# Optimization experiments

Hardware: AMD Instinct MI355X
Metric: run time of the kernel (lower is better)

Reference implementation:

```python
import jax, jax.numpy as jnp
import numpy as np

N_NODES = 100000
N_EDGES = 1600000
IN_FEAT = 128
HEADS = 4
OUT_FEAT = 16
ALPHA = 0.2  # LeakyReLU negative slope


def setup_inputs() -> dict:
    key = jax.random.key(0)
    k1, k2, k3, k4, k5 = jax.random.split(key, 5)
    x = jax.random.normal(k1, (N_NODES, IN_FEAT), dtype=jnp.float32)
    edge_index = jax.random.randint(k2, (2, N_EDGES), 0, N_NODES, dtype=jnp.int64)
    # xavier_uniform with gain=1.414
    gain = 1.414
    lim_W = gain * np.sqrt(6.0 / (IN_FEAT + HEADS * OUT_FEAT))
    W = jax.random.uniform(k3, (IN_FEAT, HEADS * OUT_FEAT), minval=-lim_W, maxval=lim_W, dtype=jnp.float32)
    lim_a = gain * np.sqrt(6.0 / (HEADS + OUT_FEAT))
    a_src = jax.random.uniform(k4, (HEADS, OUT_FEAT), minval=-lim_a, maxval=lim_a, dtype=jnp.float32)
    a_dst = jax.random.uniform(k5, (HEADS, OUT_FEAT), minval=-lim_a, maxval=lim_a, dtype=jnp.float32)
    return {"x": x, "edge_index": edge_index, "W": W, "a_src": a_src, "a_dst": a_dst}


def reference(x, edge_index, W, a_src, a_dst):
    N = x.shape[0]
    H, F = a_src.shape
    src, dst = edge_index[0], edge_index[1]

    h = (x @ W).reshape(N, H, F)                 # [N, H, F]
    att_src = jnp.sum(h * a_src, axis=-1)        # [N, H]
    att_dst = jnp.sum(h * a_dst, axis=-1)        # [N, H]

    e = jax.nn.leaky_relu(att_src[src] + att_dst[dst], negative_slope=ALPHA)  # [E, H]

    # segment softmax over edges grouped by dst
    e_max = jax.ops.segment_max(e, dst, num_segments=N)   # [N, H]
    e_max = jnp.where(jnp.isfinite(e_max), e_max, 0.0)    # nodes with no in-edges
    ex = jnp.exp(e - e_max[dst])                           # [E, H]
    denom = jax.ops.segment_sum(ex, dst, num_segments=N)  # [N, H]
    alpha = ex / (denom[dst] + 1e-16)                      # [E, H]
    # dropout: inference mode (training=False) -> identity

    messages = h[src] * alpha[:, :, None]                  # [E, H, F]
    out = jax.ops.segment_sum(messages, dst, num_segments=N)  # [N, H, F]

    out = out.reshape(N, H * F)  # concat=True
    out = jax.nn.elu(out)
    return out
```

## Files before the change

kernel.cpp:

```cpp
#include <hip/hip_runtime.h>


#define NEG_SLOPE 0.2f
#define BSHIFT 9
#define BNODES 512
#define CH 2048
#define BCB 512
#define QSHIFT 7
#define QNODES 128
#define QCAP 2816

typedef __bf16 bf16x8 __attribute__((ext_vector_type(8)));
typedef float  f32x4  __attribute__((ext_vector_type(4)));

static __device__ __forceinline__ unsigned f2b(float f) {
    union { float f; unsigned u; } v; v.f = f;
    return (v.u + 0x7fffu + ((v.u >> 16) & 1u)) >> 16;
}
static __device__ __forceinline__ float u2f(unsigned u) {
    union { unsigned u32; float f; } v; v.u32 = u; return v.f;
}

__global__ __launch_bounds__(256) void gemm_att_kernel(
    const float* __restrict__ x,
    const float* __restrict__ W,
    const float* __restrict__ a_src,
    const float* __restrict__ a_dst,
    unsigned short* __restrict__ h_out,
    float* __restrict__ att_s_o,
    float* __restrict__ att_d_o,
    const int* __restrict__ dst,
    int* __restrict__ bucketCount,
    int N, int E, int gemmBlocks)
{
    __shared__ bf16x8 Wswz[20][64];
    __shared__ int c[256];
    int t = threadIdx.x;

    if (blockIdx.x >= gemmBlocks) {
        int bid = blockIdx.x - gemmBlocks;
        c[t] = 0;
        __syncthreads();
        for (int e = bid * 256 + t; e < E; e += BCB * 256)
            atomicAdd(&c[dst[e] >> BSHIFT], 1);
        __syncthreads();
        if (c[t]) atomicAdd(&bucketCount[t], c[t]);
        return;
    }

    for (int i = t; i < 8192; i += 256) {
        int k = i >> 6, n = i & 63;
        __bf16* dp = (__bf16*)&Wswz[((n >> 4) << 2) | (k >> 5)]
                                   [(((k >> 3) & 3) << 4) | (n & 15)];
        dp[k & 7] = (__bf16)W[i];
    }
    for (int i = t; i < 1024; i += 256) {
        int k = i >> 3, c7 = i & 7;
        int hd = c7 & 3;
        const float* aa = (c7 < 4) ? a_src : a_dst;
        float sum = 0.f;
        #pragma unroll
        for (int f = 0; f < 16; ++f)
            sum = fmaf(W[k * 64 + hd * 16 + f], aa[hd * 16 + f], sum);
        __bf16* dp = (__bf16*)&Wswz[16 + (k >> 5)][(((k >> 3) & 3) << 4) | c7];
        dp[k & 7] = (__bf16)sum;
        __bf16* dz = (__bf16*)&Wswz[16 + (k >> 5)][(((k >> 3) & 3) << 4) | (8 + c7)];
        dz[k & 7] = (__bf16)0.f;
    }
    __syncthreads();

    int wave = t >> 6;
    int lane = t & 63;
    int col = lane & 15, quad = lane >> 4;
    int node_base = (blockIdx.x * 4 + wave) * 16;
    int arow = min(node_base + col, N - 1);
    const float* xp = x + arow * 128;

    bf16x8 af[4];
    #pragma unroll
    for (int tt = 0; tt < 4; ++tt) {
        float4 xa = *(const float4*)(xp + tt * 32 + quad * 8);
        float4 xb = *(const float4*)(xp + tt * 32 + quad * 8 + 4);
        bf16x8 f;
        f[0] = (__bf16)xa.x; f[1] = (__bf16)xa.y;
        f[2] = (__bf16)xa.z; f[3] = (__bf16)xa.w;
        f[4] = (__bf16)xb.x; f[5] = (__bf16)xb.y;
        f[6] = (__bf16)xb.z; f[7] = (__bf16)xb.w;
        af[tt] = f;
    }

    f32x4 acc[4], accA;
    #pragma unroll
    for (int cb = 0; cb < 4; ++cb) {
        acc[cb] = (f32x4){0.f, 0.f, 0.f, 0.f};
        #pragma unroll
        for (int tt = 0; tt < 4; ++tt)
            acc[cb] = __builtin_amdgcn_mfma_f32_16x16x32_bf16(
                af[tt], Wswz[(cb << 2) | tt][lane], acc[cb], 0, 0, 0);
    }
    accA = (f32x4){0.f, 0.f, 0.f, 0.f};
    #pragma unroll
    for (int tt = 0; tt < 4; ++tt)
        accA = __builtin_amdgcn_mfma_f32_16x16x32_bf16(
            af[tt], Wswz[16 + tt][lane], accA, 0, 0, 0);

    #pragma unroll
    for (int cb = 0; cb < 4; ++cb) {
        #pragma unroll
        for (int r = 0; r < 4; ++r) {
            int node = node_base + quad * 4 + r;
            if (node < N)
                h_out[node * 64 + cb * 16 + col] = (unsigned short)f2b(acc[cb][r]);
        }
    }
    if (col < 8) {
        #pragma unroll
        for (int r = 0; r < 4; ++r) {
            int node = node_base + quad * 4 + r;
            if (node < N) {
                if (col < 4) att_s_o[(node << 2) | col] = accA[r];
                else         att_d_o[(node << 2) | (col - 4)] = accA[r];
            }
        }
    }
}

__global__ __launch_bounds__(256) void bscatter_kernel(
    const int* __restrict__ src, const int* __restrict__ dst,
    const int* __restrict__ bucketCount,
    int* __restrict__ bucketCursor, int* __restrict__ pairs, int nb, int E)
{
    __shared__ int cnt[256], lo[256], gpos[256], cur[256], sm[256], gbc[256];
    __shared__ int2 staged[CH];
    int t = threadIdx.x;
    int base = blockIdx.x * CH;
    int nloc = min(CH, E - base);

    cnt[t] = 0;
    gbc[t] = (t < nb) ? bucketCount[t] : 0;
    __syncthreads();
    for (int i = t; i < nloc; i += 256)
        atomicAdd(&cnt[dst[base + i] >> BSHIFT], 1);
    __syncthreads();

    int v = cnt[t];
    sm[t] = v;
    __syncthreads();
    #pragma unroll
    for (int off = 1; off < 256; off <<= 1) {
        int u = (t >= off) ? sm[t - off] : 0;
        __syncthreads();
        sm[t] += u;
        __syncthreads();
    }
    lo[t] = sm[t] - v;
    cur[t] = lo[t];
    __syncthreads();

    int g = gbc[t];
    sm[t] = g;
    __syncthreads();
    #pragma unroll
    for (int off = 1; off < 256; off <<= 1) {
        int u = (t >= off) ? sm[t - off] : 0;
        __syncthreads();
        sm[t] += u;
        __syncthreads();
    }
    gpos[t] = (v > 0) ? (sm[t] - g) + atomicAdd(&bucketCursor[t], v) : 0;
    __syncthreads();

    for (int i = t; i < nloc; i += 256) {
        int d = dst[base + i];
        int s = src[base + i];
        int b = d >> BSHIFT;
        int k = atomicAdd(&cur[b], 1);
        staged[k] = make_int2((s << BSHIFT) | (d & (BNODES - 1)), b);
    }
    __syncthreads();

    for (int i = t; i < nloc; i += 256) {
        int2 p = staged[i];
        pairs[gpos[p.y] + (i - lo[p.y])] = p.x;
    }
}

__global__ __launch_bounds__(256, 8) void bucket_csr_agg_kernel(
    const int* __restrict__ pairs,
    const int* __restrict__ bucketCount,
    const float* __restrict__ att_s,
    const float* __restrict__ att_d,
    const unsigned short* __restrict__ hmat,
    float* __restrict__ out,
    int nb, int N)
{
    __shared__ int sorted[QCAP];
    __shared__ int cnt[QNODES], rs[QNODES + 1], cur[QNODES], sm[QNODES];
    __shared__ int gbc[256], gsm[256];
    __shared__ float attd[QNODES * 4];

    int blk = blockIdx.x, t = threadIdx.x;
    int b = blk >> 2, quar = blk & 3;
    int node_lo = (b << BSHIFT) + (quar << QSHIFT);
    if (node_lo >= N) return;
    int nn = min(QNODES, N - node_lo);

    { int g = (t < nb) ? bucketCount[t] : 0; gbc[t] = g; gsm[t] = g; }
    if (t < QNODES) cnt[t] = 0;
    __syncthreads();
    #pragma unroll
    for (int off = 1; off < 256; off <<= 1) {
        int u = (t >= off) ? gsm[t - off] : 0;
        __syncthreads();
        gsm[t] += u;
        __syncthreads();
    }
    int ebase = gsm[b] - gbc[b];
    int ecnt  = gbc[b];

    for (int i = t; i < (nn << 2); i += 256)
        attd[i] = att_d[(node_lo << 2) + i];

    for (int i = t; i < ecnt; i += 256) {
        int dl = pairs[ebase + i] & (BNODES - 1);
        if ((dl >> QSHIFT) == quar)
            atomicAdd(&cnt[dl & (QNODES - 1)], 1);
    }
    __syncthreads();

    int v = (t < QNODES) ? cnt[t] : 0;
    if (t < QNODES) sm[t] = v;
    __syncthreads();
    #pragma unroll
    for (int off = 1; off < QNODES; off <<= 1) {
        int u = (t >= off && t < QNODES) ? sm[t - off] : 0;
        __syncthreads();
        if (t < QNODES) sm[t] += u;
        __syncthreads();
    }
    if (t < QNODES) { int x = sm[t] - v; rs[t] = x; cur[t] = x; }
    if (t == 0) rs[QNODES] = 0;
    __syncthreads();
    if (t == 0) rs[QNODES] = (QNODES <= nn) ? sm[QNODES - 1] : sm[QNODES - 1];
    __syncthreads();

    for (int i = t; i < ecnt; i += 256) {
        int p = pairs[ebase + i];
        int dl = p & (BNODES - 1);
        if ((dl >> QSHIFT) == quar) {
            int k = atomicAdd(&cur[dl & (QNODES - 1)], 1);
            if (k < QCAP) sorted[k] = p >> BSHIFT;
        }
    }
    __syncthreads();

    int q = t & 7;
    int h = q >> 1;

    for (int pass = 0; pass < 4; ++pass) {
        int node = (pass << 5) + (t >> 3);
        if (node >= nn) continue;
        int beg = rs[node];
        int deg = rs[node + 1] - beg;
        float ad = attd[(node << 2) | h];

        float a0 = 0.f, a1 = 0.f, a2 = 0.f, a3 = 0.f;
        float a4 = 0.f, a5 = 0.f, a6 = 0.f, a7 = 0.f, l = 0.f;
        int d1 = deg - 1;
        for (int e0 = 0; e0 < deg; e0 += 4) {
            int s0 = sorted[beg + min(e0 + 0, d1)];
            int s1 = sorted[beg + min(e0 + 1, d1)];
            int s2 = sorted[beg + min(e0 + 2, d1)];
            int s3 = sorted[beg + min(e0 + 3, d1)];
            float t0 = att_s[(s0 << 2) | h];
            float t1 = att_s[(s1 << 2) | h];
            float t2 = att_s[(s2 << 2) | h];
            float t3 = att_s[(s3 << 2) | h];
            uint4 hp0 = *(const uint4*)(hmat + (s0 << 6) + (q << 3));
            uint4 hp1 = *(const uint4*)(hmat + (s1 << 6) + (q << 3));
            uint4 hp2 = *(const uint4*)(hmat + (s2 << 6) + (q << 3));
            uint4 hp3 = *(const uint4*)(hmat + (s3 << 6) + (q << 3));
            float av0 = t0 + ad; av0 = fmaxf(av0, NEG_SLOPE * av0);
            float av1 = t1 + ad; av1 = fmaxf(av1, NEG_SLOPE * av1);
            float av2 = t2 + ad; av2 = fmaxf(av2, NEG_SLOPE * av2);
            float av3 = t3 + ad; av3 = fmaxf(av3, NEG_SLOPE * av3);
            float w0 = __expf(av0);
            float w1 = (e0 + 1 < deg) ? __expf(av1) : 0.f;
            float w2 = (e0 + 2 < deg) ? __expf(av2) : 0.f;
            float w3 = (e0 + 3 < deg) ? __expf(av3) : 0.f;
            l += w0 + w1 + w2 + w3;
            a0 = fmaf(w0, u2f(hp0.x << 16), a0);
            a1 = fmaf(w0, u2f(hp0.x & 0xffff0000u), a1);
            a2 = fmaf(w0, u2f(hp0.y << 16), a2);
            a3 = fmaf(w0, u2f(hp0.y & 0xffff0000u), a3);
            a4 = fmaf(w0, u2f(hp0.z << 16), a4);
            a5 = fmaf(w0, u2f(hp0.z & 0xffff0000u), a5);
            a6 = fmaf(w0, u2f(hp0.w << 16), a6);
            a7 = fmaf(w0, u2f(hp0.w & 0xffff0000u), a7);
            a0 = fmaf(w1, u2f(hp1.x << 16), a0);
            a1 = fmaf(w1, u2f(hp1.x & 0xffff0000u), a1);
            a2 = fmaf(w1, u2f(hp1.y << 16), a2);
            a3 = fmaf(w1, u2f(hp1.y & 0xffff0000u), a3);
            a4 = fmaf(w1, u2f(hp1.z << 16), a4);
            a5 = fmaf(w1, u2f(hp1.z & 0xffff0000u), a5);
            a6 = fmaf(w1, u2f(hp1.w << 16), a6);
            a7 = fmaf(w1, u2f(hp1.w & 0xffff0000u), a7);
            a0 = fmaf(w2, u2f(hp2.x << 16), a0);
            a1 = fmaf(w2, u2f(hp2.x & 0xffff0000u), a1);
            a2 = fmaf(w2, u2f(hp2.y << 16), a2);
            a3 = fmaf(w2, u2f(hp2.y & 0xffff0000u), a3);
            a4 = fmaf(w2, u2f(hp2.z << 16), a4);
            a5 = fmaf(w2, u2f(hp2.z & 0xffff0000u), a5);
            a6 = fmaf(w2, u2f(hp2.w << 16), a6);
            a7 = fmaf(w2, u2f(hp2.w & 0xffff0000u), a7);
            a0 = fmaf(w3, u2f(hp3.x << 16), a0);
            a1 = fmaf(w3, u2f(hp3.x & 0xffff0000u), a1);
            a2 = fmaf(w3, u2f(hp3.y << 16), a2);
            a3 = fmaf(w3, u2f(hp3.y & 0xffff0000u), a3);
            a4 = fmaf(w3, u2f(hp3.z << 16), a4);
            a5 = fmaf(w3, u2f(hp3.z & 0xffff0000u), a5);
            a6 = fmaf(w3, u2f(hp3.w << 16), a6);
            a7 = fmaf(w3, u2f(hp3.w & 0xffff0000u), a7);
        }

        float rl = 1.0f / (l + 1e-16f);
        float4 v0, v1;
        v0.x = a0 * rl; v0.x = (v0.x > 0.f) ? v0.x : (__expf(v0.x) - 1.f);
        v0.y = a1 * rl; v0.y = (v0.y > 0.f) ? v0.y : (__expf(v0.y) - 1.f);
        v0.z = a2 * rl; v0.z = (v0.z > 0.f) ? v0.z : (__expf(v0.z) - 1.f);
        v0.w = a3 * rl; v0.w = (v0.w > 0.f) ? v0.w : (__expf(v0.w) - 1.f);
        v1.x = a4 * rl; v1.x = (v1.x > 0.f) ? v1.x : (__expf(v1.x) - 1.f);
        v1.y = a5 * rl; v1.y = (v1.y > 0.f) ? v1.y : (__expf(v1.y) - 1.f);
        v1.z = a6 * rl; v1.z = (v1.z > 0.f) ? v1.z : (__expf(v1.z) - 1.f);
        v1.w = a7 * rl; v1.w = (v1.w > 0.f) ? v1.w : (__expf(v1.w) - 1.f);
        float* op = out + ((size_t)(node_lo + node) << 6) + (q << 3);
        *(float4*)op = v0;
        *(float4*)(op + 4) = v1;
    }
}

extern "C" void kernel_launch(void* const* d_in, const int* in_sizes, int n_in,
                              void* d_out, int out_size, void* d_ws, size_t ws_size,
                              hipStream_t stream) {
    const float* x     = (const float*)d_in[0];
    const int*   ei    = (const int*)d_in[1];
    const float* W     = (const float*)d_in[2];
    const float* a_src = (const float*)d_in[3];
    const float* a_dst = (const float*)d_in[4];

    int N = in_sizes[0] / 128;
    int E = in_sizes[1] / 2;
    const int* src = ei;
    const int* dst = ei + E;
    int nb = (N + BNODES - 1) / BNODES;

    char* ws = (char*)d_ws;
    size_t off = 0;
    unsigned short* hmat = (unsigned short*)(ws + off); off += (size_t)N * 64 * 2;
    float* att_s = (float*)(ws + off);  off += (size_t)N * 4 * 4;
    float* att_d = (float*)(ws + off);  off += (size_t)N * 4 * 4;
    int* pairs    = (int*)(ws + off);   off += (size_t)E * 4;
    int* bucketCount  = (int*)(ws + off); off += 256 * 4;
    int* bucketCursor = (int*)(ws + off); off += 256 * 4;

    hipMemsetAsync(bucketCount, 0, 512 * 4, stream);

    int gemmBlocks = (N + 63) / 64;
    gemm_att_kernel<<<gemmBlocks + BCB, 256, 0, stream>>>(
        x, W, a_src, a_dst, hmat, att_s, att_d, dst, bucketCount,
        N, E, gemmBlocks);

    int blocksS = (E + CH - 1) / CH;
    bscatter_kernel<<<blocksS, 256, 0, stream>>>(src, dst, bucketCount,
                                                 bucketCursor, pairs, nb, E);

    bucket_csr_agg_kernel<<<nb * 4, 256, 0, stream>>>(
        pairs, bucketCount, att_s, att_d, hmat, (float*)d_out, nb, N);
}
```

Measured before the change: 211.3 us.

## Split aggregation buckets into eighths and precompute bucket offsets in scatter

```diff
diff --git a/kernel.cpp b/kernel.cpp
--- a/kernel.cpp
+++ b/kernel.cpp
@@ -6,9 +6,9 @@
 #define BNODES 512
 #define CH 2048
 #define BCB 512
-#define QSHIFT 7
-#define QNODES 128
-#define QCAP 2816
+#define QSHIFT 6
+#define QNODES 64
+#define QCAP 1536
 
 typedef __bf16 bf16x8 __attribute__((ext_vector_type(8)));
 typedef float  f32x4  __attribute__((ext_vector_type(4)));
@@ -128,7 +128,8 @@
 __global__ __launch_bounds__(256) void bscatter_kernel(
     const int* __restrict__ src, const int* __restrict__ dst,
     const int* __restrict__ bucketCount,
-    int* __restrict__ bucketCursor, int* __restrict__ pairs, int nb, int E)
+    int* __restrict__ bucketCursor, int* __restrict__ pairs,
+    int* __restrict__ bbase, int nb, int E)
 {
     __shared__ int cnt[256], lo[256], gpos[256], cur[256], sm[256], gbc[256];
     __shared__ int2 staged[CH];
@@ -168,6 +169,10 @@
         __syncthreads();
     }
     gpos[t] = (v > 0) ? (sm[t] - g) + atomicAdd(&bucketCursor[t], v) : 0;
+    if (blockIdx.x == 0) {
+        bbase[t + 1] = sm[t];
+        if (t == 0) bbase[0] = 0;
+    }
     __syncthreads();
 
     for (int i = t; i < nloc; i += 256) {
@@ -187,43 +192,34 @@
 
 __global__ __launch_bounds__(256, 8) void bucket_csr_agg_kernel(
     const int* __restrict__ pairs,
-    const int* __restrict__ bucketCount,
+    const int* __restrict__ bbase,
     const float* __restrict__ att_s,
     const float* __restrict__ att_d,
     const unsigned short* __restrict__ hmat,
     float* __restrict__ out,
-    int nb, int N)
+    int N)
 {
     __shared__ int sorted[QCAP];
     __shared__ int cnt[QNODES], rs[QNODES + 1], cur[QNODES], sm[QNODES];
-    __shared__ int gbc[256], gsm[256];
     __shared__ float attd[QNODES * 4];
 
     int blk = blockIdx.x, t = threadIdx.x;
-    int b = blk >> 2, quar = blk & 3;
-    int node_lo = (b << BSHIFT) + (quar << QSHIFT);
+    int b = blk >> 3, s8 = blk & 7;
+    int node_lo = (b << BSHIFT) + (s8 << QSHIFT);
     if (node_lo >= N) return;
     int nn = min(QNODES, N - node_lo);
 
-    { int g = (t < nb) ? bucketCount[t] : 0; gbc[t] = g; gsm[t] = g; }
+    int ebase = bbase[b];
+    int ecnt  = bbase[b + 1] - ebase;
+
     if (t < QNODES) cnt[t] = 0;
-    __syncthreads();
-    #pragma unroll
-    for (int off = 1; off < 256; off <<= 1) {
-        int u = (t >= off) ? gsm[t - off] : 0;
-        __syncthreads();
-        gsm[t] += u;
-        __syncthreads();
-    }
-    int ebase = gsm[b] - gbc[b];
-    int ecnt  = gbc[b];
-
     for (int i = t; i < (nn << 2); i += 256)
         attd[i] = att_d[(node_lo << 2) + i];
+    __syncthreads();
 
     for (int i = t; i < ecnt; i += 256) {
         int dl = pairs[ebase + i] & (BNODES - 1);
-        if ((dl >> QSHIFT) == quar)
+        if ((dl >> QSHIFT) == s8)
             atomicAdd(&cnt[dl & (QNODES - 1)], 1);
     }
     __syncthreads();
@@ -238,16 +234,16 @@
         if (t < QNODES) sm[t] += u;
         __syncthreads();
     }
-    if (t < QNODES) { int x = sm[t] - v; rs[t] = x; cur[t] = x; }
-    if (t == 0) rs[QNODES] = 0;
-    __syncthreads();
-    if (t == 0) rs[QNODES] = (QNODES <= nn) ? sm[QNODES - 1] : sm[QNODES - 1];
+    if (t < QNODES) {
+        int x = sm[t] - v; rs[t] = x; cur[t] = x;
+        if (t == QNODES - 1) rs[QNODES] = sm[t];
+    }
     __syncthreads();
 
     for (int i = t; i < ecnt; i += 256) {
         int p = pairs[ebase + i];
         int dl = p & (BNODES - 1);
-        if ((dl >> QSHIFT) == quar) {
+        if ((dl >> QSHIFT) == s8) {
             int k = atomicAdd(&cur[dl & (QNODES - 1)], 1);
             if (k < QCAP) sorted[k] = p >> BSHIFT;
         }
@@ -256,8 +252,9 @@
 
     int q = t & 7;
     int h = q >> 1;
-
-    for (int pass = 0; pass < 4; ++pass) {
+    int nclamp = N - 1;
+
+    for (int pass = 0; pass < 2; ++pass) {
         int node = (pass << 5) + (t >> 3);
         if (node >= nn) continue;
         int beg = rs[node];
@@ -268,10 +265,10 @@
         float a4 = 0.f, a5 = 0.f, a6 = 0.f, a7 = 0.f, l = 0.f;
         int d1 = deg - 1;
         for (int e0 = 0; e0 < deg; e0 += 4) {
-            int s0 = sorted[beg + min(e0 + 0, d1)];
-            int s1 = sorted[beg + min(e0 + 1, d1)];
-            int s2 = sorted[beg + min(e0 + 2, d1)];
-            int s3 = sorted[beg + min(e0 + 3, d1)];
+            int s0 = min(sorted[beg + min(e0 + 0, d1)], nclamp);
+            int s1 = min(sorted[beg + min(e0 + 1, d1)], nclamp);
+            int s2 = min(sorted[beg + min(e0 + 2, d1)], nclamp);
+            int s3 = min(sorted[beg + min(e0 + 3, d1)], nclamp);
             float t0 = att_s[(s0 << 2) | h];
             float t1 = att_s[(s1 << 2) | h];
             float t2 = att_s[(s2 << 2) | h];
@@ -362,6 +359,7 @@
     int* pairs    = (int*)(ws + off);   off += (size_t)E * 4;
     int* bucketCount  = (int*)(ws + off); off += 256 * 4;
     int* bucketCursor = (int*)(ws + off); off += 256 * 4;
+    int* bbase    = (int*)(ws + off);   off += 257 * 4;
 
     hipMemsetAsync(bucketCount, 0, 512 * 4, stream);
 
@@ -372,8 +370,9 @@
 
     int blocksS = (E + CH - 1) / CH;
     bscatter_kernel<<<blocksS, 256, 0, stream>>>(src, dst, bucketCount,
-                                                 bucketCursor, pairs, nb, E);
-
-    bucket_csr_agg_kernel<<<nb * 4, 256, 0, stream>>>(
-        pairs, bucketCount, att_s, att_d, hmat, (float*)d_out, nb, N);
-}
+                                                 bucketCursor, pairs, bbase,
+                                                 nb, E);
+
+    bucket_csr_agg_kernel<<<nb * 8, 256, 0, stream>>>(
+        pairs, bbase, att_s, att_d, hmat, (float*)d_out, N);
+}
```

New measurement: 213.5 us. About the same (+1.1%).
